# Performance work log

Hardware: AMD Instinct MI355X
Metric: run time of the kernel (lower is better)

The kernel has to match this reference:

```python
import jax, jax.numpy as jnp
import numpy as np

B = 65536
HID = 128
OUT = 10


def setup_inputs() -> dict:
    key = jax.random.key(0)
    ks = jax.random.split(key, 6)
    x = jax.random.normal(ks[0], (B, 784), dtype=jnp.float32)
    conv_w = jax.random.normal(ks[1], (3, 3), dtype=jnp.float32)
    # torch Linear(676,128): weight [128,676], bias [128]
    w1 = jax.random.normal(ks[2], (HID, 26 * 26), dtype=jnp.float32) * (1.0 / np.sqrt(26 * 26))
    b1 = jax.random.normal(ks[3], (HID,), dtype=jnp.float32) * 0.01
    w2 = jax.random.normal(ks[4], (OUT, HID), dtype=jnp.float32) * (1.0 / np.sqrt(HID))
    b2 = jax.random.normal(ks[5], (OUT,), dtype=jnp.float32) * 0.01
    return {"x": x, "conv_w": conv_w, "w1": w1, "b1": b1, "w2": w2, "b2": b2}


def reference(x, conv_w, w1, b1, w2, b2):
    b = x.shape[0]
    img = x.reshape(b, 1, 28, 28)                      # NCHW, single channel
    kern = conv_w.reshape(1, 1, 3, 3)                  # OIHW
    # valid 3x3 cross-correlation (matches the elementwise-multiply-and-sum loop)
    conv = jax.lax.conv_general_dilated(
        img, kern, window_strides=(1, 1), padding="VALID",
        dimension_numbers=("NCHW", "OIHW", "NCHW"))   # [B,1,26,26]
    feat = conv.reshape(b, 26 * 26)
    h = jax.nn.relu(feat @ w1.T + b1)                  # [B,128]
    return h @ w2.T + b2                               # [B,10]
```

## Files before the change

### kernel.cpp

```cpp
#include <hip/hip_runtime.h>
#include <hip/hip_bf16.h>

#define BATCH  65536
#define KREAL  784
#define BK     64
#define NCHUNK 13
#define HID    128
#define NOUT   10
#define BM     64
#define NTHR   256

using f32x4  = __attribute__((ext_vector_type(4))) float;
using short8 = __attribute__((ext_vector_type(8))) short;
using f4     = __attribute__((ext_vector_type(4))) float;

__device__ inline short f2b(float f) {
    union { __hip_bfloat16 h; short s; } u;
    u.h = __float2bfloat16(f);
    return u.s;
}

#define GLDS16(gp, lp) \
    __builtin_amdgcn_global_load_lds((const __attribute__((address_space(1))) void*)(gp), \
                                     (__attribute__((address_space(3))) void*)(lp), 16, 0, 0)

#define NWB (NCHUNK*HID*BK)
#define NW2 (4*4*16*8)

__global__ void prep_kernel(const float* __restrict__ conv_w,
                            const float* __restrict__ w1,
                            const float* __restrict__ w2,
                            unsigned short* __restrict__ weff_sw,
                            unsigned short* __restrict__ w2f)
{
    int idx = blockIdx.x * 256 + threadIdx.x;
    if (idx < NWB) {
        int ic  = idx >> 13;
        int rem = idx & 8191;
        int r   = rem >> 6;
        int cc  = rem & 63;
        int g   = (cc >> 3) ^ (r & 7);
        int k   = ic * BK + g * 8 + (cc & 7);
        float acc = 0.f;
        if (k < KREAL) {
            int rr = k / 28, c = k - rr * 28;
            #pragma unroll
            for (int di = 0; di < 3; ++di) {
                int i = rr - di;
                if (i >= 0 && i < 26) {
                    #pragma unroll
                    for (int dj = 0; dj < 3; ++dj) {
                        int j = c - dj;
                        if (j >= 0 && j < 26)
                            acc = fmaf(w1[r * 676 + i * 26 + j], conv_w[di * 3 + dj], acc);
                    }
                }
            }
        }
        weff_sw[idx] = (unsigned short)f2b(acc);
    } else {
        int k2 = idx - NWB;
        if (k2 < NW2) {
            int e  = k2 & 7;
            int lo = (k2 >> 3) & 15;
            int hi = (k2 >> 7) & 3;
            int kk = k2 >> 9;
            float v = (lo < NOUT) ? w2[lo * HID + kk * 32 + hi * 8 + e] : 0.f;
            w2f[k2] = (unsigned short)f2b(v);
        }
    }
}

__global__ __launch_bounds__(NTHR, 2)
void fused_mlp_kernel(const float* __restrict__ x,
                      const float* __restrict__ b1,
                      const float* __restrict__ b2,
                      const unsigned short* __restrict__ weff_sw,
                      const unsigned short* __restrict__ w2f,
                      float* __restrict__ out)
{
    __shared__ __align__(16) unsigned char smem[65536];
    float*          bufA0 = (float*)smem;
    float*          bufA1 = (float*)(smem + 16384);
    unsigned short* bufB0 = (unsigned short*)(smem + 32768);
    unsigned short* bufB1 = (unsigned short*)(smem + 49152);
    unsigned short* ldsH  = (unsigned short*)smem;

    const int tid  = threadIdx.x;
    const int wv   = tid >> 6;
    const int lane = tid & 63;
    const int lo   = lane & 15;
    const int hi   = lane >> 4;
    const int row0 = blockIdx.x * BM;
    const int wr0  = wv * 16;

    f32x4 acc[8];
    #pragma unroll
    for (int t = 0; t < 8; ++t) acc[t] = (f32x4){0.f, 0.f, 0.f, 0.f};

    const char* abase = (const char*)(x + (long)(row0 + wr0 + hi) * KREAL);
    auto stageA = [&](int ic, float* dst) {
        #pragma unroll
        for (int j = 0; j < 4; ++j) {
            int sg = lo ^ (j * 4 + hi);
            int ce = ic * BK + sg * 4;
            int cb = (ce < KREAL) ? ce : 0;
            GLDS16(abase + (long)j * 4 * KREAL * 4 + cb * 4,
                   (char*)dst + (wr0 + j * 4) * 256);
        }
    };
    auto stageB = [&](int ic, unsigned short* dst) {
        const char* src = (const char*)(weff_sw + (long)ic * (HID * BK));
        #pragma unroll
        for (int j = 0; j < 4; ++j)
            GLDS16(src + wv * 4096 + j * 1024 + lane * 16,
                   (char*)dst + wv * 4096 + j * 1024);
    };

    stageA(0, bufA0);
    stageB(0, bufB0);

    #pragma unroll
    for (int ic = 0; ic < NCHUNK; ++ic) {
        const float*          Ac = (ic & 1) ? bufA1 : bufA0;
        const unsigned short* Bc = (ic & 1) ? bufB1 : bufB0;
        if (ic + 1 < NCHUNK) {
            stageA(ic + 1, (ic & 1) ? bufA0 : bufA1);
            stageB(ic + 1, (ic & 1) ? bufB0 : bufB1);
            asm volatile("s_waitcnt vmcnt(8)" ::: "memory");
        } else {
            asm volatile("s_waitcnt vmcnt(0)" ::: "memory");
        }
        __builtin_amdgcn_s_barrier();
        __builtin_amdgcn_sched_barrier(0);

        const int r = wr0 + lo;
        #pragma unroll
        for (int kk = 0; kk < 2; ++kk) {
            const int G = kk * 4 + hi;
            f4 a0 = *(const f4*)((const char*)Ac + r * 256 + ((( 2 * G    ) ^ lo) << 4));
            f4 a1 = *(const f4*)((const char*)Ac + r * 256 + (((2 * G + 1) ^ lo) << 4));
            short8 af;
            #pragma unroll
            for (int e = 0; e < 4; ++e) {
                af[e]     = f2b(a0[e]);
                af[4 + e] = f2b(a1[e]);
            }
            #pragma unroll
            for (int t = 0; t < 8; ++t) {
                const int ob = t * 16 + lo;
                short8 bfrag = *(const short8*)&Bc[ob * BK + ((G ^ (ob & 7)) << 3)];
                acc[t] = __builtin_amdgcn_mfma_f32_16x16x32_bf16(af, bfrag, acc[t], 0, 0, 0);
            }
        }
        if (ic + 1 < NCHUNK) {
            __builtin_amdgcn_sched_barrier(0);
            __builtin_amdgcn_s_barrier();
        }
    }

    #pragma unroll
    for (int t = 0; t < 8; ++t) {
        float bias = b1[t * 16 + lo];
        #pragma unroll
        for (int j = 0; j < 4; ++j) {
            float hv = acc[t][j] + bias;
            hv = hv > 0.f ? hv : 0.f;
            int rloc = wr0 + hi * 4 + j;
            int col  = t * 16 + lo;
            int g    = col >> 3, e = col & 7;
            ldsH[rloc * HID + ((g ^ (rloc & 7)) << 3) + e] = (unsigned short)f2b(hv);
        }
    }

    f32x4 acc2 = (f32x4){0.f, 0.f, 0.f, 0.f};
    #pragma unroll
    for (int kk = 0; kk < 4; ++kk) {
        int r = wr0 + lo;
        int g = kk * 4 + hi;
        short8 ha = *(const short8*)&ldsH[r * HID + ((g ^ (r & 7)) << 3)];
        short8 wb = *(const short8*)(w2f + (((kk * 4 + hi) * 16 + lo) << 3));
        acc2 = __builtin_amdgcn_mfma_f32_16x16x32_bf16(ha, wb, acc2, 0, 0, 0);
    }
    if (lo < NOUT) {
        float bb = b2[lo];
        #pragma unroll
        for (int j = 0; j < 4; ++j) {
            int grow = row0 + wr0 + hi * 4 + j;
            out[grow * NOUT + lo] = acc2[j] + bb;
        }
    }
}

extern "C" void kernel_launch(void* const* d_in, const int* in_sizes, int n_in,
                              void* d_out, int out_size, void* d_ws, size_t ws_size,
                              hipStream_t stream)
{
    const float* x      = (const float*)d_in[0];
    const float* conv_w = (const float*)d_in[1];
    const float* w1     = (const float*)d_in[2];
    const float* b1     = (const float*)d_in[3];
    const float* w2     = (const float*)d_in[4];
    const float* b2     = (const float*)d_in[5];
    float* out = (float*)d_out;

    unsigned short* weff_sw = (unsigned short*)d_ws;
    unsigned short* w2f     = weff_sw + NWB;

    const int prep_total = NWB + NW2;
    prep_kernel<<<(prep_total + 255) / 256, 256, 0, stream>>>(conv_w, w1, w2, weff_sw, w2f);
    fused_mlp_kernel<<<BATCH / BM, NTHR, 0, stream>>>(x, b1, b2, weff_sw, w2f, out);
}
```

Measured before the change: 44.64 us.

## Convert A tile to bf16 in registers before LDS, double block size

Switches x staging from direct global-to-LDS fp32 copies to register loads that are converted to bf16 and written swizzled into LDS. This halves A tile LDS footprint and removes per-MFMA conversion work. Blocks grow to 128 rows and 512 threads with higher occupancy bounds, and output rows are staged through LDS for vectorized stores. In exchange, the global load latency for A is now exposed within each iteration through a full vmcnt(0) wait before the LDS write.

```diff
diff --git a/kernel.cpp b/kernel.cpp
--- a/kernel.cpp
+++ b/kernel.cpp
@@ -7,11 +7,12 @@
 #define NCHUNK 13
 #define HID    128
 #define NOUT   10
-#define BM     64
-#define NTHR   256
+#define BM     128
+#define NTHR   512
 
 using f32x4  = __attribute__((ext_vector_type(4))) float;
 using short8 = __attribute__((ext_vector_type(8))) short;
+using short4v= __attribute__((ext_vector_type(4))) short;
 using f4     = __attribute__((ext_vector_type(4))) float;
 
 __device__ inline short f2b(float f) {
@@ -71,7 +72,7 @@
     }
 }
 
-__global__ __launch_bounds__(NTHR, 2)
+__global__ __launch_bounds__(NTHR, 4)
 void fused_mlp_kernel(const float* __restrict__ x,
                       const float* __restrict__ b1,
                       const float* __restrict__ b2,
@@ -80,11 +81,12 @@
                       float* __restrict__ out)
 {
     __shared__ __align__(16) unsigned char smem[65536];
-    float*          bufA0 = (float*)smem;
-    float*          bufA1 = (float*)(smem + 16384);
-    unsigned short* bufB0 = (unsigned short*)(smem + 32768);
-    unsigned short* bufB1 = (unsigned short*)(smem + 49152);
+    unsigned short* ldsA0 = (unsigned short*)smem;
+    unsigned short* ldsA1 = (unsigned short*)(smem + 16384);
+    unsigned short* ldsB0 = (unsigned short*)(smem + 32768);
+    unsigned short* ldsB1 = (unsigned short*)(smem + 49152);
     unsigned short* ldsH  = (unsigned short*)smem;
+    float*          outS  = (float*)(smem + 49152);
 
     const int tid  = threadIdx.x;
     const int wv   = tid >> 6;
@@ -99,53 +101,53 @@
     for (int t = 0; t < 8; ++t) acc[t] = (f32x4){0.f, 0.f, 0.f, 0.f};
 
     const char* abase = (const char*)(x + (long)(row0 + wr0 + hi) * KREAL);
-    auto stageA = [&](int ic, float* dst) {
+    f4 av[4];
+    auto issueA = [&](int ic) {
         #pragma unroll
         for (int j = 0; j < 4; ++j) {
-            int sg = lo ^ (j * 4 + hi);
-            int ce = ic * BK + sg * 4;
-            int cb = (ce < KREAL) ? ce : 0;
-            GLDS16(abase + (long)j * 4 * KREAL * 4 + cb * 4,
-                   (char*)dst + (wr0 + j * 4) * 256);
+            int ce = ic * BK + lo * 4;
+            int cb = (ce + 4 <= KREAL) ? ce : 0;
+            av[j] = *(const f4*)(abase + (long)j * 4 * KREAL * 4 + (long)cb * 4);
+        }
+    };
+    auto writeA = [&](unsigned short* dstA) {
+        #pragma unroll
+        for (int j = 0; j < 4; ++j) {
+            int r = wr0 + j * 4 + hi;
+            short4v c;
+            c[0] = f2b(av[j][0]); c[1] = f2b(av[j][1]);
+            c[2] = f2b(av[j][2]); c[3] = f2b(av[j][3]);
+            int byteoff = r * 128 + ((((lo >> 1) ^ (r & 7)) << 4)) + ((lo & 1) << 3);
+            *(short4v*)((char*)dstA + byteoff) = c;
         }
     };
     auto stageB = [&](int ic, unsigned short* dst) {
         const char* src = (const char*)(weff_sw + (long)ic * (HID * BK));
-        #pragma unroll
-        for (int j = 0; j < 4; ++j)
-            GLDS16(src + wv * 4096 + j * 1024 + lane * 16,
-                   (char*)dst + wv * 4096 + j * 1024);
+        GLDS16(src + wv * 2048 + lane * 16,        (char*)dst + wv * 2048);
+        GLDS16(src + wv * 2048 + 1024 + lane * 16, (char*)dst + wv * 2048 + 1024);
     };
 
-    stageA(0, bufA0);
-    stageB(0, bufB0);
+    issueA(0);
+    stageB(0, ldsB0);
+    asm volatile("s_waitcnt vmcnt(0)" ::: "memory");
+    __builtin_amdgcn_sched_barrier(0);
+    writeA(ldsA0);
+    __builtin_amdgcn_s_barrier();
+    __builtin_amdgcn_sched_barrier(0);
 
     #pragma unroll
     for (int ic = 0; ic < NCHUNK; ++ic) {
-        const float*          Ac = (ic & 1) ? bufA1 : bufA0;
-        const unsigned short* Bc = (ic & 1) ? bufB1 : bufB0;
+        const unsigned short* Ac = (ic & 1) ? ldsA1 : ldsA0;
+        const unsigned short* Bc = (ic & 1) ? ldsB1 : ldsB0;
         if (ic + 1 < NCHUNK) {
-            stageA(ic + 1, (ic & 1) ? bufA0 : bufA1);
-            stageB(ic + 1, (ic & 1) ? bufB0 : bufB1);
-            asm volatile("s_waitcnt vmcnt(8)" ::: "memory");
-        } else {
-            asm volatile("s_waitcnt vmcnt(0)" ::: "memory");
-        }
-        __builtin_amdgcn_s_barrier();
-        __builtin_amdgcn_sched_barrier(0);
-
+            issueA(ic + 1);
+            stageB(ic + 1, (ic & 1) ? ldsB0 : ldsB1);
+        }
         const int r = wr0 + lo;
         #pragma unroll
         for (int kk = 0; kk < 2; ++kk) {
             const int G = kk * 4 + hi;
-            f4 a0 = *(const f4*)((const char*)Ac + r * 256 + ((( 2 * G    ) ^ lo) << 4));
-            f4 a1 = *(const f4*)((const char*)Ac + r * 256 + (((2 * G + 1) ^ lo) << 4));
-            short8 af;
-            #pragma unroll
-            for (int e = 0; e < 4; ++e) {
-                af[e]     = f2b(a0[e]);
-                af[4 + e] = f2b(a1[e]);
-            }
+            short8 af = *(const short8*)((const char*)Ac + r * 128 + ((G ^ (r & 7)) << 4));
             #pragma unroll
             for (int t = 0; t < 8; ++t) {
                 const int ob = t * 16 + lo;
@@ -155,9 +157,18 @@
         }
         if (ic + 1 < NCHUNK) {
             __builtin_amdgcn_sched_barrier(0);
+            asm volatile("s_waitcnt vmcnt(0)" ::: "memory");
+            __builtin_amdgcn_sched_barrier(0);
+            writeA((ic & 1) ? ldsA0 : ldsA1);
+            __builtin_amdgcn_sched_barrier(0);
             __builtin_amdgcn_s_barrier();
-        }
-    }
+            __builtin_amdgcn_sched_barrier(0);
+        }
+    }
+
+    __builtin_amdgcn_sched_barrier(0);
+    __builtin_amdgcn_s_barrier();
+    __builtin_amdgcn_sched_barrier(0);
 
     #pragma unroll
     for (int t = 0; t < 8; ++t) {
@@ -182,13 +193,16 @@
         short8 wb = *(const short8*)(w2f + (((kk * 4 + hi) * 16 + lo) << 3));
         acc2 = __builtin_amdgcn_mfma_f32_16x16x32_bf16(ha, wb, acc2, 0, 0, 0);
     }
+    float* os = outS + wv * 160;
     if (lo < NOUT) {
         float bb = b2[lo];
         #pragma unroll
-        for (int j = 0; j < 4; ++j) {
-            int grow = row0 + wr0 + hi * 4 + j;
-            out[grow * NOUT + lo] = acc2[j] + bb;
-        }
+        for (int j = 0; j < 4; ++j)
+            os[(hi * 4 + j) * NOUT + lo] = acc2[j] + bb;
+    }
+    if (lane < 40) {
+        f4 v = *(const f4*)&os[lane * 4];
+        *(f4*)(out + (long)(row0 + wr0) * NOUT + lane * 4) = v;
     }
 }
 
```

Result: faster. 43.67 us (-2.2%).
